# Kernel optimization log

Measured on AMD Instinct MI355X. Metric: run time of the kernel, lower is better.

## Reference

```python
import jax, jax.numpy as jnp
import numpy as np
from jax import lax

M, G = 16, 4
INP = 256
OUP = 256
K = 3
EPS = 1e-5


def _weightnet(x, gap_vec, fc1_w, fc1_b, fc2_w, inp, oup, stride):
    # x: [B, inp, H, W], gap_vec: [B, 16]
    B, _, H, W = x.shape
    a = jax.nn.sigmoid(gap_vec @ fc1_w.T + fc1_b)          # [B, M*oup]
    groups = G * oup                                        # 1024
    out_pg = (oup * inp * K * K) // groups                  # 576
    in_pg = (M * oup) // groups                             # 4
    a = a.reshape(B, groups, in_pg)
    w2 = fc2_w.reshape(groups, out_pg, in_pg)
    # grouped 1x1 conv generating per-sample conv weights
    xw = jnp.einsum('bgi,goi->bgo', a, w2)                  # [B, groups, out_pg]
    xw = xw.reshape(B * oup, inp, K, K)                     # per-sample kernels
    xr = x.reshape(1, B * inp, H, W)
    out = lax.conv_general_dilated(
        xr, xw, (stride, stride), [(1, 1), (1, 1)],
        dimension_numbers=('NCHW', 'OIHW', 'NCHW'),
        feature_group_count=B)
    return out.reshape(B, oup, out.shape[2], out.shape[3])


def _bn(x, g, b, m, v):
    scale = (g / jnp.sqrt(v + EPS))[:, None, None]
    return (x - m[:, None, None]) * scale + b[:, None, None]


def setup_inputs() -> dict:
    key = jax.random.key(0)
    ks = jax.random.split(key, 20)
    d = {}
    d['x'] = jax.random.normal(ks[0], (32, 256, 56, 56), jnp.float32)
    d['reduce_w'] = jax.random.normal(ks[1], (16, 256), jnp.float32) * 0.05
    d['reduce_b'] = jax.random.normal(ks[2], (16,), jnp.float32) * 0.05
    d['w1_fc1_w'] = jax.random.normal(ks[3], (4096, 16), jnp.float32) * 0.05
    d['w1_fc1_b'] = jax.random.normal(ks[4], (4096,), jnp.float32) * 0.05
    d['w1_fc2_w'] = jax.random.normal(ks[5], (589824, 4), jnp.float32) * 0.05
    d['bn1_g'] = jax.random.uniform(ks[6], (256,), jnp.float32) + 0.5
    d['bn1_b'] = jax.random.normal(ks[7], (256,), jnp.float32) * 0.05
    d['bn1_m'] = jax.random.normal(ks[8], (256,), jnp.float32) * 0.05
    d['bn1_v'] = jax.random.uniform(ks[9], (256,), jnp.float32) + 0.5
    d['w2_fc1_w'] = jax.random.normal(ks[10], (4096, 16), jnp.float32) * 0.05
    d['w2_fc1_b'] = jax.random.normal(ks[11], (4096,), jnp.float32) * 0.05
    d['w2_fc2_w'] = jax.random.normal(ks[12], (589824, 4), jnp.float32) * 0.05
    d['bn2_g'] = jax.random.uniform(ks[13], (256,), jnp.float32) + 0.5
    d['bn2_b'] = jax.random.normal(ks[14], (256,), jnp.float32) * 0.05
    d['bn2_m'] = jax.random.normal(ks[15], (256,), jnp.float32) * 0.05
    d['bn2_v'] = jax.random.uniform(ks[16], (256,), jnp.float32) + 0.5
    return d


def reference(x, reduce_w, reduce_b, w1_fc1_w, w1_fc1_b, w1_fc2_w,
              bn1_g, bn1_b, bn1_m, bn1_v,
              w2_fc1_w, w2_fc1_b, w2_fc2_w,
              bn2_g, bn2_b, bn2_m, bn2_v):
    # global average pool -> reduce 1x1 conv
    gap = x.mean(axis=(2, 3))                       # [B, in_planes]
    gap = gap @ reduce_w.T + reduce_b               # [B, 16]
    out = _weightnet(x, gap, w1_fc1_w, w1_fc1_b, w1_fc2_w, INP, OUP, 1)
    out = jax.nn.relu(_bn(out, bn1_g, bn1_b, bn1_m, bn1_v))
    out = _weightnet(out, gap, w2_fc1_w, w2_fc1_b, w2_fc2_w, OUP, OUP, 1)
    out = _bn(out, bn2_g, bn2_b, bn2_m, bn2_v)
    out = out + x                                   # identity shortcut (stride=1, in==out)
    return jax.nn.relu(out)
```

## Files before the change

### kernel.cpp

```cpp
#include <hip/hip_runtime.h>

typedef short bf16x8 __attribute__((ext_vector_type(8)));
typedef float f32x4 __attribute__((ext_vector_type(4)));

#define EPSV 1e-5f
#define BNUM 32
#define CH 256
#define HW 3136
#define PXT 3684
#define NCHUNK 32
#define PERB_SHORTS (NCHUNK*PXT*8)
#define WB_PERB 589824

__device__ __forceinline__ unsigned short f2bf(float f) {
  unsigned int u = __float_as_uint(f);
  u += 0x7fffu + ((u >> 16) & 1u);
  return (unsigned short)(u >> 16);
}

__device__ __forceinline__ void gld16(const void* g, void* l) {
  __builtin_amdgcn_global_load_lds((const __attribute__((address_space(1))) void*)g,
                                   (__attribute__((address_space(3))) void*)l,
                                   16, 0, 0);
}

__global__ void k_gapc(const float* __restrict__ x, float* __restrict__ gapc) {
  int bc = blockIdx.x;
  const float4* p4 = (const float4*)(x + (size_t)bc * HW);
  int t = threadIdx.x;
  float s = 0.f;
  for (int i = t; i < 784; i += 256) {
    float4 v = p4[i];
    s += v.x + v.y + v.z + v.w;
  }
  for (int off = 32; off; off >>= 1) s += __shfl_down(s, off, 64);
  __shared__ float red[4];
  int lane = t & 63, wv = t >> 6;
  if (lane == 0) red[wv] = s;
  __syncthreads();
  if (t == 0) gapc[bc] = (red[0] + red[1] + red[2] + red[3]) * (1.f / 3136.f);
}

__global__ void k_gap16(const float* __restrict__ gapc, const float* __restrict__ rw,
                        const float* __restrict__ rb, float* __restrict__ g16) {
  int b = blockIdx.x;
  int t = threadIdx.x;
  int j = t >> 5;
  int c0 = t & 31;
  const float* gc = gapc + b * 256;
  const float* w = rw + j * 256;
  float s = 0.f;
#pragma unroll
  for (int k = 0; k < 8; ++k) s += gc[c0 + k * 32] * w[c0 + k * 32];
  for (int off = 16; off; off >>= 1) s += __shfl_down(s, off, 32);
  if (c0 == 0) g16[b * 16 + j] = s + rb[j];
}

__global__ void k_act(const float* __restrict__ g16,
                      const float* __restrict__ w1w, const float* __restrict__ w1b,
                      const float* __restrict__ w2w, const float* __restrict__ w2b,
                      float* __restrict__ a1, float* __restrict__ a2) {
  int idx = blockIdx.x * 256 + threadIdx.x;
  int which = idx >> 17;
  int r = idx & 131071;
  int b = r >> 12, m = r & 4095;
  const float* w = (which ? w2w : w1w) + m * 16;
  float s = which ? w2b[m] : w1b[m];
  const float* g = g16 + b * 16;
#pragma unroll
  for (int j = 0; j < 16; ++j) s += g[j] * w[j];
  float out = 1.f / (1.f + __expf(-s));
  (which ? a2 : a1)[r] = out;
}

__global__ void k_zero(unsigned short* __restrict__ xp1, unsigned short* __restrict__ xp2) {
  int bc = blockIdx.x;
  int t = threadIdx.x;
  uint4 z = {0u, 0u, 0u, 0u};
  for (int wbuf = 0; wbuf < 2; ++wbuf) {
    unsigned short* base = (wbuf ? xp2 : xp1) + (size_t)bc * (PXT * 8);
    uint4* p = (uint4*)base;
    if (t < 123) p[t] = z;
    p[3370 + t] = z;
    if (t < 58) p[3626 + t] = z;
    if (t < 56) {
      int e = 64 + (t + 1) * 58 + 57;
      p[e] = z;
      p[e + 1] = z;
    }
  }
}

__global__ void k_xpad(const float* __restrict__ x, unsigned short* __restrict__ xp) {
  int y = blockIdx.x, ch = blockIdx.y, b = blockIdx.z;
  int l = threadIdx.x;
  if (l >= 56) return;
  const float* src = x + ((size_t)(b * 256 + ch * 8)) * HW + y * 56 + l;
  ushort4 lo, hi;
  lo.x = f2bf(src[0 * HW]); lo.y = f2bf(src[1 * HW]);
  lo.z = f2bf(src[2 * HW]); lo.w = f2bf(src[3 * HW]);
  hi.x = f2bf(src[4 * HW]); hi.y = f2bf(src[5 * HW]);
  hi.z = f2bf(src[6 * HW]); hi.w = f2bf(src[7 * HW]);
  unsigned short* dst = xp + ((size_t)(b * NCHUNK + ch)) * (PXT * 8)
                           + (size_t)(64 + (y + 1) * 58 + (l + 1)) * 8;
  *(ushort4*)dst = lo;
  *(ushort4*)(dst + 4) = hi;
}

__global__ void k_wgen(const float* __restrict__ a, const float4* __restrict__ w2,
                       unsigned short* __restrict__ wb) {
  int og = blockIdx.x & 63, bg = blockIdx.x >> 6;
  int t = threadIdx.x;
  for (int bi = 0; bi < 4; ++bi) {
    int b = bg * 4 + bi;
    const float* ab = a + b * 4096;
    unsigned short* wbb = wb + (size_t)b * WB_PERB;
    for (int it = 0; it < 36; ++it) {
      int wi = it * 256 + t;
      int oc_l = wi / 2304;
      int r = wi - oc_l * 2304;
      int ic = r / 9;
      int k9 = r - ic * 9;
      int kh = k9 / 3;
      int kw = k9 - kh * 3;
      int oc = og * 4 + oc_l;
      int g = oc * 4 + (ic >> 6);
      int o = (ic & 63) * 9 + k9;
      float4 w4 = w2[g * 576 + o];
      float4 a4 = *(const float4*)(ab + g * 4);
      float s = w4.x * a4.x + w4.y * a4.y + w4.z * a4.z + w4.w * a4.w;
      int s_ = ic >> 5, kc_ = (ic >> 3) & 3, icl = ic & 7;
      int ocg_ = oc >> 7, ocl_ = oc & 127;
      wbb[(size_t)((kh * 8 + s_) * 2 + ocg_) * 12288 + kc_ * 3072 + ocl_ * 24 + kw * 8 + icl]
          = f2bf(s);
    }
  }
}

__global__ __launch_bounds__(256, 2)
void k_conv(const unsigned short* __restrict__ xpad,
            const unsigned short* __restrict__ wbuf,
            const float* __restrict__ bgp, const float* __restrict__ bbp,
            const float* __restrict__ bmp, const float* __restrict__ bvp,
            const float* __restrict__ resid,
            unsigned short* __restrict__ outpad,
            float* __restrict__ outf,
            const int mode) {
  __shared__ unsigned short sW[2][12288];
  __shared__ unsigned short sX[2][8192];

  const int tid = threadIdx.x;
  const int lane = tid & 63;
  const int wv = tid >> 6;
  const int wocg = wv >> 1;
  const int wpxg = wv & 1;
  const int ocl = lane & 15;
  const int kc = lane >> 4;

  int rid = blockIdx.x;
  int xcd = rid & 7;
  int j = rid >> 3;
  int b = xcd + 8 * (j / 30);
  int slot = j % 30;
  int bocg = slot & 1;
  int p0 = 58 + (slot >> 1) * 224;

  const unsigned short* xb = xpad + (size_t)b * PERB_SHORTS + 64 * 8;
  const unsigned short* wbb = wbuf + (size_t)b * WB_PERB + bocg * 12288;

  f32x4 acc[4][7];
#pragma unroll
  for (int i = 0; i < 4; ++i)
#pragma unroll
    for (int k = 0; k < 7; ++k)
      acc[i][k] = (f32x4){0.f, 0.f, 0.f, 0.f};

  auto STAGE = [&](int t, int buf) {
    int s = t / 3;
    int kh = t - s * 3;
    const unsigned short* wsrc = wbb + (size_t)(kh * 8 + s) * 24576;
#pragma unroll
    for (int i = 0; i < 6; ++i) {
      int seg = wv * 6 + i;
      gld16(wsrc + seg * 512 + lane * 8, &sW[buf][seg * 512]);
    }
    int q0 = p0 + kh * 58 - 59;
    const unsigned short* xs = xb + ((long)(s * 4 + wv) * PXT + q0) * 8;
#pragma unroll
    for (int i = 0; i < 4; ++i)
      gld16(xs + (i * 64 + lane) * 8, &sX[buf][wv * 2048 + i * 512]);
  };

  STAGE(0, 0);
  int cur = 0;
  for (int t = 0; t < 24; ++t) {
    if (t + 1 < 24) {
      STAGE(t + 1, cur ^ 1);
      asm volatile("s_waitcnt vmcnt(10)" ::: "memory");
    } else {
      asm volatile("s_waitcnt vmcnt(0)" ::: "memory");
    }
    __builtin_amdgcn_s_barrier();
#pragma unroll
    for (int kw = 0; kw < 3; ++kw) {
      bf16x8 af[4], bfr[7];
#pragma unroll
      for (int fm = 0; fm < 4; ++fm)
        af[fm] = *(const bf16x8*)&sW[cur][kc * 3072 + (wocg * 64 + fm * 16 + ocl) * 24 + kw * 8];
#pragma unroll
      for (int fn = 0; fn < 7; ++fn)
        bfr[fn] = *(const bf16x8*)&sX[cur][kc * 2048 + (wpxg * 112 + fn * 16 + ocl + kw) * 8];
      __builtin_amdgcn_s_setprio(1);
#pragma unroll
      for (int fm = 0; fm < 4; ++fm)
#pragma unroll
        for (int fn = 0; fn < 7; ++fn)
          acc[fm][fn] = __builtin_amdgcn_mfma_f32_16x16x32_bf16(af[fm], bfr[fn], acc[fm][fn], 0, 0, 0);
      __builtin_amdgcn_s_setprio(0);
    }
    __builtin_amdgcn_s_barrier();
    cur ^= 1;
  }

  float* scb = (float*)&sX[0][0];
  if (tid < 128) {
    int oc = bocg * 128 + tid;
    float sc = bgp[oc] * rsqrtf(bvp[oc] + EPSV);
    scb[tid] = sc;
    scb[128 + tid] = bbp[oc] - bmp[oc] * sc;
  }
  __syncthreads();

  const int dpb = wpxg * 112 + ocl;
  if (mode == 1) {
#pragma unroll
    for (int fn = 0; fn < 7; ++fn) {
      int pp = p0 + dpb + fn * 16;
      int py = pp / 58;
      int px = pp - py * 58;
      if (py < 1 || py > 56 || px < 1 || px > 56) continue;
#pragma unroll
      for (int fm = 0; fm < 4; ++fm) {
        int loc = wocg * 64 + fm * 16 + kc * 4;
        f32x4 v = acc[fm][fn];
        ushort4 w;
        w.x = f2bf(fmaxf(v[0] * scb[loc + 0] + scb[128 + loc + 0], 0.f));
        w.y = f2bf(fmaxf(v[1] * scb[loc + 1] + scb[128 + loc + 1], 0.f));
        w.z = f2bf(fmaxf(v[2] * scb[loc + 2] + scb[128 + loc + 2], 0.f));
        w.w = f2bf(fmaxf(v[3] * scb[loc + 3] + scb[128 + loc + 3], 0.f));
        int ocg_g = bocg * 128 + loc;
        *(ushort4*)&outpad[((size_t)(b * NCHUNK + (ocg_g >> 3))) * (PXT * 8)
                           + (size_t)(64 + pp) * 8 + (ocg_g & 7)] = w;
      }
    }
  } else {
#pragma unroll
    for (int fn = 0; fn < 7; ++fn) {
      int pp = p0 + dpb + fn * 16;
      int py = pp / 58;
      int px = pp - py * 58;
      if (py < 1 || py > 56 || px < 1 || px > 56) continue;
      int obase = (py - 1) * 56 + (px - 1);
#pragma unroll
      for (int fm = 0; fm < 4; ++fm) {
        int loc = wocg * 64 + fm * 16 + kc * 4;
        f32x4 v = acc[fm][fn];
#pragma unroll
        for (int r = 0; r < 4; ++r) {
          int oc = bocg * 128 + loc + r;
          size_t oi = ((size_t)(b * CH + oc)) * HW + obase;
          float tv = v[r] * scb[loc + r] + scb[128 + loc + r] + resid[oi];
          outf[oi] = fmaxf(tv, 0.f);
        }
      }
    }
  }
}

#define OFF_XP1 ((size_t)0)
#define XP_BYTES ((size_t)BNUM * PERB_SHORTS * 2)
#define OFF_XP2 (OFF_XP1 + XP_BYTES)
#define OFF_WB  (OFF_XP2 + XP_BYTES)
#define WB_BYTES ((size_t)BNUM * WB_PERB * 2)
#define OFF_GAPC (OFF_WB + WB_BYTES)
#define OFF_G16  (OFF_GAPC + 32768)
#define OFF_A1   (OFF_G16 + 2048)
#define OFF_A2   (OFF_A1 + 524288)

extern "C" void kernel_launch(void* const* d_in, const int* in_sizes, int n_in,
                              void* d_out, int out_size, void* d_ws, size_t ws_size,
                              hipStream_t stream) {
  (void)in_sizes; (void)n_in; (void)out_size; (void)ws_size;
  const float* x        = (const float*)d_in[0];
  const float* reduce_w = (const float*)d_in[1];
  const float* reduce_b = (const float*)d_in[2];
  const float* w1fc1w   = (const float*)d_in[3];
  const float* w1fc1b   = (const float*)d_in[4];
  const float* w1fc2w   = (const float*)d_in[5];
  const float* bn1g     = (const float*)d_in[6];
  const float* bn1b     = (const float*)d_in[7];
  const float* bn1m     = (const float*)d_in[8];
  const float* bn1v     = (const float*)d_in[9];
  const float* w2fc1w   = (const float*)d_in[10];
  const float* w2fc1b   = (const float*)d_in[11];
  const float* w2fc2w   = (const float*)d_in[12];
  const float* bn2g     = (const float*)d_in[13];
  const float* bn2b     = (const float*)d_in[14];
  const float* bn2m     = (const float*)d_in[15];
  const float* bn2v     = (const float*)d_in[16];

  char* ws = (char*)d_ws;
  unsigned short* xp1 = (unsigned short*)(ws + OFF_XP1);
  unsigned short* xp2 = (unsigned short*)(ws + OFF_XP2);
  unsigned short* wb  = (unsigned short*)(ws + OFF_WB);
  float* gapc = (float*)(ws + OFF_GAPC);
  float* g16  = (float*)(ws + OFF_G16);
  float* a1   = (float*)(ws + OFF_A1);
  float* a2   = (float*)(ws + OFF_A2);
  float* outf = (float*)d_out;

  k_gapc<<<BNUM * CH, 256, 0, stream>>>(x, gapc);
  k_gap16<<<BNUM, 512, 0, stream>>>(gapc, reduce_w, reduce_b, g16);
  k_act<<<1024, 256, 0, stream>>>(g16, w1fc1w, w1fc1b, w2fc1w, w2fc1b, a1, a2);
  k_zero<<<1024, 256, 0, stream>>>(xp1, xp2);
  k_xpad<<<dim3(56, NCHUNK, BNUM), 64, 0, stream>>>(x, xp1);

  k_wgen<<<512, 256, 0, stream>>>(a1, (const float4*)w1fc2w, wb);
  k_conv<<<960, 256, 0, stream>>>(xp1, wb, bn1g, bn1b, bn1m, bn1v,
                                  nullptr, xp2, nullptr, 1);
  k_wgen<<<512, 256, 0, stream>>>(a2, (const float4*)w2fc2w, wb);
  k_conv<<<960, 256, 0, stream>>>(xp2, wb, bn2g, bn2b, bn2m, bn2v,
                                  x, nullptr, outf, 2);
}
```

Measured before the change: 410.5 us.

## Fuse GAP into pad kernel, reuse fc2 weights in wgen, stage X once per slice

The global-average-pool reduction now runs inside the bf16 padding kernel through wave shuffles and atomics, so the separate pass over x is gone and the 1/HW scale moves into gap16. The weight generator loads each fc2 weight once and applies it to four batch samples, instead of reloading it per sample. The conv kernel now stages the input tile for all three kh rows once per channel slice in a single buffer and double-buffers only the weights. This cuts global loads, but input staging is no longer overlapped with compute and the float atomics make the pooled sums order-dependent.

```diff
diff --git a/kernel.cpp b/kernel.cpp
--- a/kernel.cpp
+++ b/kernel.cpp
@@ -22,23 +22,6 @@
   __builtin_amdgcn_global_load_lds((const __attribute__((address_space(1))) void*)g,
                                    (__attribute__((address_space(3))) void*)l,
                                    16, 0, 0);
-}
-
-__global__ void k_gapc(const float* __restrict__ x, float* __restrict__ gapc) {
-  int bc = blockIdx.x;
-  const float4* p4 = (const float4*)(x + (size_t)bc * HW);
-  int t = threadIdx.x;
-  float s = 0.f;
-  for (int i = t; i < 784; i += 256) {
-    float4 v = p4[i];
-    s += v.x + v.y + v.z + v.w;
-  }
-  for (int off = 32; off; off >>= 1) s += __shfl_down(s, off, 64);
-  __shared__ float red[4];
-  int lane = t & 63, wv = t >> 6;
-  if (lane == 0) red[wv] = s;
-  __syncthreads();
-  if (t == 0) gapc[bc] = (red[0] + red[1] + red[2] + red[3]) * (1.f / 3136.f);
 }
 
 __global__ void k_gap16(const float* __restrict__ gapc, const float* __restrict__ rw,
@@ -53,7 +36,7 @@
 #pragma unroll
   for (int k = 0; k < 8; ++k) s += gc[c0 + k * 32] * w[c0 + k * 32];
   for (int off = 16; off; off >>= 1) s += __shfl_down(s, off, 32);
-  if (c0 == 0) g16[b * 16 + j] = s + rb[j];
+  if (c0 == 0) g16[b * 16 + j] = s * (1.f / 3136.f) + rb[j];
 }
 
 __global__ void k_act(const float* __restrict__ g16,
@@ -91,48 +74,59 @@
   }
 }
 
-__global__ void k_xpad(const float* __restrict__ x, unsigned short* __restrict__ xp) {
+__global__ void k_xpad(const float* __restrict__ x, unsigned short* __restrict__ xp,
+                       float* __restrict__ gapc) {
   int y = blockIdx.x, ch = blockIdx.y, b = blockIdx.z;
   int l = threadIdx.x;
-  if (l >= 56) return;
-  const float* src = x + ((size_t)(b * 256 + ch * 8)) * HW + y * 56 + l;
-  ushort4 lo, hi;
-  lo.x = f2bf(src[0 * HW]); lo.y = f2bf(src[1 * HW]);
-  lo.z = f2bf(src[2 * HW]); lo.w = f2bf(src[3 * HW]);
-  hi.x = f2bf(src[4 * HW]); hi.y = f2bf(src[5 * HW]);
-  hi.z = f2bf(src[6 * HW]); hi.w = f2bf(src[7 * HW]);
-  unsigned short* dst = xp + ((size_t)(b * NCHUNK + ch)) * (PXT * 8)
-                           + (size_t)(64 + (y + 1) * 58 + (l + 1)) * 8;
-  *(ushort4*)dst = lo;
-  *(ushort4*)(dst + 4) = hi;
+  bool act = (l < 56);
+  int lc = act ? l : 0;
+  const float* src = x + ((size_t)(b * 256 + ch * 8)) * HW + y * 56 + lc;
+  float v[8];
+#pragma unroll
+  for (int k = 0; k < 8; ++k) v[k] = act ? src[k * HW] : 0.f;
+  if (act) {
+    ushort4 lo, hi;
+    lo.x = f2bf(v[0]); lo.y = f2bf(v[1]); lo.z = f2bf(v[2]); lo.w = f2bf(v[3]);
+    hi.x = f2bf(v[4]); hi.y = f2bf(v[5]); hi.z = f2bf(v[6]); hi.w = f2bf(v[7]);
+    unsigned short* dst = xp + ((size_t)(b * NCHUNK + ch)) * (PXT * 8)
+                             + (size_t)(64 + (y + 1) * 58 + (l + 1)) * 8;
+    *(ushort4*)dst = lo;
+    *(ushort4*)(dst + 4) = hi;
+  }
+#pragma unroll
+  for (int k = 0; k < 8; ++k) {
+    float s = v[k];
+    for (int off = 32; off; off >>= 1) s += __shfl_down(s, off, 64);
+    if (l == 0) atomicAdd(&gapc[b * 256 + ch * 8 + k], s);
+  }
 }
 
 __global__ void k_wgen(const float* __restrict__ a, const float4* __restrict__ w2,
                        unsigned short* __restrict__ wb) {
   int og = blockIdx.x & 63, bg = blockIdx.x >> 6;
   int t = threadIdx.x;
-  for (int bi = 0; bi < 4; ++bi) {
-    int b = bg * 4 + bi;
-    const float* ab = a + b * 4096;
-    unsigned short* wbb = wb + (size_t)b * WB_PERB;
-    for (int it = 0; it < 36; ++it) {
-      int wi = it * 256 + t;
-      int oc_l = wi / 2304;
-      int r = wi - oc_l * 2304;
-      int ic = r / 9;
-      int k9 = r - ic * 9;
-      int kh = k9 / 3;
-      int kw = k9 - kh * 3;
-      int oc = og * 4 + oc_l;
-      int g = oc * 4 + (ic >> 6);
-      int o = (ic & 63) * 9 + k9;
-      float4 w4 = w2[g * 576 + o];
-      float4 a4 = *(const float4*)(ab + g * 4);
+  for (int it = 0; it < 36; ++it) {
+    int wi = it * 256 + t;
+    int oc_l = wi / 2304;
+    int r = wi - oc_l * 2304;
+    int ic = r / 9;
+    int k9 = r - ic * 9;
+    int kh = k9 / 3;
+    int kw = k9 - kh * 3;
+    int oc = og * 4 + oc_l;
+    int g = oc * 4 + (ic >> 6);
+    int o = (ic & 63) * 9 + k9;
+    float4 w4 = w2[g * 576 + o];
+    int s_ = ic >> 5, kc_ = (ic >> 3) & 3, icl = ic & 7;
+    int ocg_ = oc >> 7, ocl_ = oc & 127;
+    size_t off = (size_t)((kh * 8 + s_) * 2 + ocg_) * 12288 + kc_ * 3072 + ocl_ * 24
+               + kw * 8 + icl;
+#pragma unroll
+    for (int bi = 0; bi < 4; ++bi) {
+      int b = bg * 4 + bi;
+      float4 a4 = *(const float4*)(a + b * 4096 + g * 4);
       float s = w4.x * a4.x + w4.y * a4.y + w4.z * a4.z + w4.w * a4.w;
-      int s_ = ic >> 5, kc_ = (ic >> 3) & 3, icl = ic & 7;
-      int ocg_ = oc >> 7, ocl_ = oc & 127;
-      wbb[(size_t)((kh * 8 + s_) * 2 + ocg_) * 12288 + kc_ * 3072 + ocl_ * 24 + kw * 8 + icl]
-          = f2bf(s);
+      wb[(size_t)b * WB_PERB + off] = f2bf(s);
     }
   }
 }
@@ -147,7 +141,7 @@
             float* __restrict__ outf,
             const int mode) {
   __shared__ unsigned short sW[2][12288];
-  __shared__ unsigned short sX[2][8192];
+  __shared__ unsigned short sX[12288];
 
   const int tid = threadIdx.x;
   const int lane = tid & 63;
@@ -175,7 +169,7 @@
     for (int k = 0; k < 7; ++k)
       acc[i][k] = (f32x4){0.f, 0.f, 0.f, 0.f};
 
-  auto STAGE = [&](int t, int buf) {
+  auto STAGE_W = [&](int t, int buf) {
     int s = t / 3;
     int kh = t - s * 3;
     const unsigned short* wsrc = wbb + (size_t)(kh * 8 + s) * 24576;
@@ -184,45 +178,54 @@
       int seg = wv * 6 + i;
       gld16(wsrc + seg * 512 + lane * 8, &sW[buf][seg * 512]);
     }
-    int q0 = p0 + kh * 58 - 59;
-    const unsigned short* xs = xb + ((long)(s * 4 + wv) * PXT + q0) * 8;
-#pragma unroll
-    for (int i = 0; i < 4; ++i)
-      gld16(xs + (i * 64 + lane) * 8, &sX[buf][wv * 2048 + i * 512]);
   };
-
-  STAGE(0, 0);
+  auto STAGE_X = [&](int s) {
+    const unsigned short* xs = xb + ((long)(s * 4 + wv) * PXT + p0 - 59) * 8;
+#pragma unroll
+    for (int i = 0; i < 6; ++i)
+      gld16(xs + (i * 64 + lane) * 8, &sX[wv * 3072 + i * 512]);
+  };
+
+  STAGE_X(0);
+  STAGE_W(0, 0);
   int cur = 0;
-  for (int t = 0; t < 24; ++t) {
-    if (t + 1 < 24) {
-      STAGE(t + 1, cur ^ 1);
-      asm volatile("s_waitcnt vmcnt(10)" ::: "memory");
-    } else {
-      asm volatile("s_waitcnt vmcnt(0)" ::: "memory");
-    }
+  for (int s8 = 0; s8 < 8; ++s8) {
+    asm volatile("s_waitcnt vmcnt(0)" ::: "memory");
     __builtin_amdgcn_s_barrier();
 #pragma unroll
-    for (int kw = 0; kw < 3; ++kw) {
-      bf16x8 af[4], bfr[7];
-#pragma unroll
-      for (int fm = 0; fm < 4; ++fm)
-        af[fm] = *(const bf16x8*)&sW[cur][kc * 3072 + (wocg * 64 + fm * 16 + ocl) * 24 + kw * 8];
-#pragma unroll
-      for (int fn = 0; fn < 7; ++fn)
-        bfr[fn] = *(const bf16x8*)&sX[cur][kc * 2048 + (wpxg * 112 + fn * 16 + ocl + kw) * 8];
-      __builtin_amdgcn_s_setprio(1);
-#pragma unroll
-      for (int fm = 0; fm < 4; ++fm)
+    for (int kh = 0; kh < 3; ++kh) {
+      int t = s8 * 3 + kh;
+      if (t + 1 < 24) {
+        STAGE_W(t + 1, cur ^ 1);
+        asm volatile("s_waitcnt vmcnt(6)" ::: "memory");
+      } else {
+        asm volatile("s_waitcnt vmcnt(0)" ::: "memory");
+      }
+      __builtin_amdgcn_s_barrier();
+#pragma unroll
+      for (int kw = 0; kw < 3; ++kw) {
+        bf16x8 af[4], bfr[7];
+#pragma unroll
+        for (int fm = 0; fm < 4; ++fm)
+          af[fm] = *(const bf16x8*)&sW[cur][kc * 3072 + (wocg * 64 + fm * 16 + ocl) * 24 + kw * 8];
 #pragma unroll
         for (int fn = 0; fn < 7; ++fn)
-          acc[fm][fn] = __builtin_amdgcn_mfma_f32_16x16x32_bf16(af[fm], bfr[fn], acc[fm][fn], 0, 0, 0);
-      __builtin_amdgcn_s_setprio(0);
-    }
-    __builtin_amdgcn_s_barrier();
-    cur ^= 1;
-  }
-
-  float* scb = (float*)&sX[0][0];
+          bfr[fn] = *(const bf16x8*)&sX[kc * 3072 + (kh * 58 + wpxg * 112 + fn * 16 + ocl + kw) * 8];
+        __builtin_amdgcn_s_setprio(1);
+#pragma unroll
+        for (int fm = 0; fm < 4; ++fm)
+#pragma unroll
+          for (int fn = 0; fn < 7; ++fn)
+            acc[fm][fn] = __builtin_amdgcn_mfma_f32_16x16x32_bf16(af[fm], bfr[fn], acc[fm][fn], 0, 0, 0);
+        __builtin_amdgcn_s_setprio(0);
+      }
+      __builtin_amdgcn_s_barrier();
+      if (kh == 2 && s8 + 1 < 8) STAGE_X(s8 + 1);
+      cur ^= 1;
+    }
+  }
+
+  float* scb = (float*)&sX[0];
   if (tid < 128) {
     int oc = bocg * 128 + tid;
     float sc = bgp[oc] * rsqrtf(bvp[oc] + EPSV);
@@ -319,11 +322,11 @@
   float* a2   = (float*)(ws + OFF_A2);
   float* outf = (float*)d_out;
 
-  k_gapc<<<BNUM * CH, 256, 0, stream>>>(x, gapc);
+  hipMemsetAsync(gapc, 0, 32 * 256 * 4, stream);
+  k_zero<<<1024, 256, 0, stream>>>(xp1, xp2);
+  k_xpad<<<dim3(56, NCHUNK, BNUM), 64, 0, stream>>>(x, xp1, gapc);
   k_gap16<<<BNUM, 512, 0, stream>>>(gapc, reduce_w, reduce_b, g16);
   k_act<<<1024, 256, 0, stream>>>(g16, w1fc1w, w1fc1b, w2fc1w, w2fc1b, a1, a2);
-  k_zero<<<1024, 256, 0, stream>>>(xp1, xp2);
-  k_xpad<<<dim3(56, NCHUNK, BNUM), 64, 0, stream>>>(x, xp1);
 
   k_wgen<<<512, 256, 0, stream>>>(a1, (const float4*)w1fc2w, wb);
   k_conv<<<960, 256, 0, stream>>>(xp1, wb, bn1g, bn1b, bn1m, bn1v,
```

Result: slower. 472.0 us (+15.0%).
